# Kernel optimization log

Measured on AMD Instinct MI355X. Metric: run time of the kernel, lower is better.

The kernel has to match this reference:

```python
import jax, jax.numpy as jnp
import numpy as np
import math

B, C, H, W = 8, 512, 32, 32
NH = 8           # num_heads
G = 32           # group norm groups
EPS = 1e-6


def group_norm(x, gamma, beta, groups=G, eps=EPS):
    # x: [B, C, H, W]
    b, c, h, w = x.shape
    xr = x.reshape(b, groups, c // groups, h, w)
    mu = xr.mean(axis=(2, 3, 4), keepdims=True)
    var = xr.var(axis=(2, 3, 4), keepdims=True)
    xn = ((xr - mu) * jax.lax.rsqrt(var + eps)).reshape(b, c, h, w)
    return xn * gamma[None, :, None, None] + beta[None, :, None, None]


def conv2d(x, w, b, pad):
    y = jax.lax.conv_general_dilated(
        x, w, window_strides=(1, 1), padding=[(pad, pad), (pad, pad)],
        dimension_numbers=("NCHW", "OIHW", "NCHW"))
    return y + b[None, :, None, None]


def setup_inputs() -> dict:
    key = jax.random.key(0)
    ks = jax.random.split(key, 20)
    def n(k, shape, s=0.02):
        return jax.random.normal(k, shape, dtype=jnp.float32) * s
    f32 = jnp.float32
    return {
        "hidden_states": jax.random.normal(ks[0], (B, C, H, W), dtype=f32),
        "pre_g": jnp.ones(C, f32), "pre_b": jnp.zeros(C, f32),
        "norm_g": jnp.ones(C, f32), "norm_b": jnp.zeros(C, f32),
        "post_g": jnp.ones(C, f32), "post_b": jnp.zeros(C, f32),
        "pos_emb": n(ks[1], (1, C, 32, 32)),
        "wq": n(ks[2], (C, C)), "wk": n(ks[3], (C, C)), "wv": n(ks[4], (C, C)),
        "wq0": n(ks[5], (C // 2, C)), "wq1": n(ks[6], (C // 2, C)),
        "wk0": n(ks[7], (C // 2, C)), "wk1": n(ks[8], (C // 2, C)),
        "wv0": n(ks[9], (C // 2, C)), "wv1": n(ks[10], (C // 2, C)),
        "sa_w1": n(ks[11], (C // 8, C, 1, 1)), "sa_b1": jnp.zeros(C // 8, f32),
        "sa_w2": n(ks[12], (C // 8, C // 8, 3, 3)), "sa_b2": jnp.zeros(C // 8, f32),
        "sa_w3": n(ks[13], (1, C // 8, 1, 1)), "sa_b3": jnp.zeros(1, f32),
        "ff_w1": n(ks[14], (C, 2 * C)), "ff_b1": jnp.zeros(C, f32),
        "ff_w2": n(ks[15], (C, C)), "ff_b2": jnp.zeros(C, f32),
        "out_w": n(ks[16], (C, C)), "out_b": jnp.zeros(C, f32),
    }


def reference(hidden_states, pre_g, pre_b, norm_g, norm_b, post_g, post_b,
              pos_emb, wq, wk, wv, wq0, wq1, wk0, wk1, wv0, wv1,
              sa_w1, sa_b1, sa_w2, sa_b2, sa_w3, sa_b3,
              ff_w1, ff_b1, ff_w2, ff_b2, out_w, out_b):
    b, c, h, w = hidden_states.shape
    S = h * w
    residual = hidden_states
    x = group_norm(hidden_states, pre_g, pre_b)
    # H == W == 32: bilinear interpolation of pos_emb to its own size is identity
    x = x + pos_emb
    # conv-based sigmoid spatial gate
    s1 = jax.nn.silu(conv2d(x, sa_w1, sa_b1, 0))
    s2 = jax.nn.silu(conv2d(s1, sa_w2, sa_b2, 1))
    spatial_weights = jax.nn.sigmoid(conv2d(s2, sa_w3, sa_b3, 0))  # [B,1,H,W]
    spatial_enhanced = x * spatial_weights
    # standard attention path (self-attention: encoder states = normed tokens)
    sh = group_norm(x, norm_g, norm_b).reshape(b, c, S).transpose(0, 2, 1)  # [B,S,C]
    enc = sh
    hd = c // NH
    def split_heads(t):
        return t.reshape(b, S, NH, hd).transpose(0, 2, 1, 3)  # [B,NH,S,hd]
    qh = split_heads(sh @ wq.T)
    kh = split_heads(enc @ wk.T)
    vh = split_heads(enc @ wv.T)
    scores = jnp.einsum("bhqd,bhkd->bhqk", qh, kh) / math.sqrt(hd)
    probs = jax.nn.softmax(scores, axis=-1)
    standard_out = jnp.einsum("bhqk,bhkd->bhqd", probs, vh)
    standard_out = standard_out.transpose(0, 2, 1, 3).reshape(b, S, c)
    # multi-scale attention paths over the spatially gated features (single head)
    msh = spatial_enhanced.reshape(b, c, S).transpose(0, 2, 1)  # [B,S,C]
    parts = []
    for wqm, wkm, wvm in ((wq0, wk0, wv0), (wq1, wk1, wv1)):
        qm = msh @ wqm.T      # [B,S,C/2]
        km = enc @ wkm.T
        vm = enc @ wvm.T
        sc = jnp.einsum("bqd,bkd->bqk", qm, km) / math.sqrt(qm.shape[-1])
        parts.append(jnp.einsum("bqk,bkd->bqd", jax.nn.softmax(sc, axis=-1), vm))
    multi_out = jnp.concatenate(parts, axis=-1)            # [B,S,C]
    combined = jnp.concatenate([standard_out, multi_out], axis=-1)  # [B,S,2C]
    fused = jax.nn.silu(combined @ ff_w1.T + ff_b1) @ ff_w2.T + ff_b2  # dropout = eval
    final = fused @ out_w.T + out_b
    final = final.transpose(0, 2, 1).reshape(b, c, h, w)
    final = group_norm(final, post_g, post_b)
    return final + residual
```

## Files before the change

kernel.cpp:

```cpp
#include <hip/hip_runtime.h>

typedef unsigned short u16;
typedef unsigned long long u64;
typedef __attribute__((ext_vector_type(8))) short s8v;
typedef __attribute__((ext_vector_type(4))) short s4v;
typedef __attribute__((ext_vector_type(4))) float f4v;

#define LOG2E 1.4426950408889634f

__device__ __forceinline__ float b2f(u16 u) {
  union { unsigned u; float f; } x; x.u = ((unsigned)u) << 16; return x.f;
}
__device__ __forceinline__ u16 f2b(float f) {
  union { float f; unsigned u; } x; x.f = f;
  unsigned r = x.u + 0x7fffu + ((x.u >> 16) & 1u);
  return (u16)(r >> 16);
}
__device__ __forceinline__ unsigned cvtpk(float lo, float hi) {
  unsigned r;
  asm("v_cvt_pk_bf16_f32 %0, %1, %2" : "=v"(r) : "v"(lo), "v"(hi));
  return r;
}

#define MFMA16(a, b, c) __builtin_amdgcn_mfma_f32_16x16x32_bf16((a), (b), (c), 0, 0, 0)

__device__ __forceinline__ void gload16(const void* g, void* l) {
  __builtin_amdgcn_global_load_lds(
      (const __attribute__((address_space(1))) unsigned*)g,
      (__attribute__((address_space(3))) unsigned*)l, 16, 0, 0);
}

struct Segs {
  const float* src[14];
  int cum[15];
  float scl[14];
};

__global__ __launch_bounds__(256) void castk(Segs sg, u16* __restrict__ dst) {
  int gid = (blockIdx.x * 256 + threadIdx.x) * 4;
  if (gid >= sg.cum[14]) return;
  int s = 0;
  while (gid >= sg.cum[s + 1]) ++s;
  const float* sp = sg.src[s] + (gid - sg.cum[s]);
  float sc = sg.scl[s];
  f4v v = *(const f4v*)sp;
  s4v o;
  o[0] = (short)f2b(v[0] * sc); o[1] = (short)f2b(v[1] * sc);
  o[2] = (short)f2b(v[2] * sc); o[3] = (short)f2b(v[3] * sc);
  *(s4v*)(dst + gid) = o;
}

__global__ __launch_bounds__(256) void gn1_k(
    const float* __restrict__ hs, const float* __restrict__ pg, const float* __restrict__ pb,
    const float* __restrict__ pos, float* __restrict__ x,
    float* __restrict__ mu2, float* __restrict__ rs2)
{
  int bid = blockIdx.x;
  int b = bid >> 5, g = bid & 31;
  int tid = threadIdx.x, l = tid & 63, w = tid >> 6;
  const float* src = hs + ((size_t)b * 512 + g * 16) * 1024;
  const float* pp = pos + (size_t)(g * 16) * 1024;
  float* dst = x + ((size_t)b * 512 + g * 16) * 1024;
  f4v vals[16];
  float sum = 0.f, sq = 0.f;
#pragma unroll
  for (int i = 0; i < 16; ++i) {
    int idx = tid + i * 256;
    vals[i] = *(const f4v*)(src + (size_t)idx * 4);
    f4v v = vals[i];
    sum += v[0] + v[1] + v[2] + v[3];
    sq += v[0] * v[0] + v[1] * v[1] + v[2] * v[2] + v[3] * v[3];
  }
  __shared__ float red[8];
#pragma unroll
  for (int off = 1; off < 64; off <<= 1) { sum += __shfl_xor(sum, off); sq += __shfl_xor(sq, off); }
  if (l == 0) { red[w * 2] = sum; red[w * 2 + 1] = sq; }
  __syncthreads();
  float S = red[0] + red[2] + red[4] + red[6];
  float Q = red[1] + red[3] + red[5] + red[7];
  float mean = S * (1.f / 16384.f);
  float var = Q * (1.f / 16384.f) - mean * mean;
  float rstd = rsqrtf(var + 1e-6f);
  __syncthreads();
  float sum2 = 0.f, sq2 = 0.f;
#pragma unroll
  for (int i = 0; i < 16; ++i) {
    int idx = tid + i * 256;
    int c = idx >> 8;
    float gam = pg[g * 16 + c], bet = pb[g * 16 + c];
    f4v v = vals[i];
    f4v pe = *(const f4v*)(pp + (size_t)idx * 4);
    f4v o;
#pragma unroll
    for (int j = 0; j < 4; ++j) o[j] = (v[j] - mean) * rstd * gam + bet + pe[j];
    *(f4v*)(dst + (size_t)idx * 4) = o;
    sum2 += o[0] + o[1] + o[2] + o[3];
    sq2 += o[0] * o[0] + o[1] * o[1] + o[2] * o[2] + o[3] * o[3];
  }
#pragma unroll
  for (int off = 1; off < 64; off <<= 1) { sum2 += __shfl_xor(sum2, off); sq2 += __shfl_xor(sq2, off); }
  if (l == 0) { red[w * 2] = sum2; red[w * 2 + 1] = sq2; }
  __syncthreads();
  if (tid == 0) {
    float S2 = red[0] + red[2] + red[4] + red[6];
    float Q2 = red[1] + red[3] + red[5] + red[7];
    float m2 = S2 * (1.f / 16384.f);
    float v2 = Q2 * (1.f / 16384.f) - m2 * m2;
    mu2[b * 32 + g] = m2;
    rs2[b * 32 + g] = rsqrtf(v2 + 1e-6f);
  }
}

__global__ __launch_bounds__(256) void trans_gn2(
    const float* __restrict__ x, const float* __restrict__ mu2, const float* __restrict__ rs2,
    const float* __restrict__ ng, const float* __restrict__ nb,
    u16* __restrict__ xt, u16* __restrict__ sh)
{
  __shared__ float lds[512 * 17];
  int st = blockIdx.x, b = blockIdx.y;
  int tid = threadIdx.x;
  const float* xp = x + (size_t)b * 512 * 1024 + st * 16;
#pragma unroll
  for (int i = 0; i < 8; ++i) {
    int idx = tid + i * 256;
    int c = idx >> 2, sq = idx & 3;
    f4v v = *(const f4v*)(xp + (size_t)c * 1024 + sq * 4);
#pragma unroll
    for (int j = 0; j < 4; ++j) lds[c * 17 + sq * 4 + j] = v[j];
  }
  __syncthreads();
  int s = tid & 15, cb0 = (tid >> 4) * 32;
  size_t token = (size_t)b * 1024 + st * 16 + s;
  float m0 = mu2[b * 32 + (cb0 >> 4)], m1 = mu2[b * 32 + (cb0 >> 4) + 1];
  float r0 = rs2[b * 32 + (cb0 >> 4)], r1 = rs2[b * 32 + (cb0 >> 4) + 1];
#pragma unroll
  for (int q = 0; q < 4; ++q) {
    s8v ox, os;
#pragma unroll
    for (int j = 0; j < 8; ++j) {
      int cj = q * 8 + j;
      int c = cb0 + cj;
      float v = lds[c * 17 + s];
      ox[j] = (short)f2b(v);
      float mm = (cj < 16) ? m0 : m1;
      float rr = (cj < 16) ? r0 : r1;
      os[j] = (short)f2b((v - mm) * rr * ng[c] + nb[c]);
    }
    *(s8v*)(xt + token * 512 + cb0 + q * 8) = ox;
    *(s8v*)(sh + token * 512 + cb0 + q * 8) = os;
  }
}

template <int BM, int BN, bool SILU, bool OUT32, bool BIAS>
__global__ __launch_bounds__(256, 2) void gemm_k(
    const u16* __restrict__ A, int lda,
    const u16* __restrict__ Bw, int ldb,
    void* __restrict__ Cp, int ldc,
    const float* __restrict__ bias, int K, int ntx)
{
  constexpr int WMT = BM / 2, WNT = BN / 2, MF = WMT / 16, NF = WNT / 16;
  __shared__ u16 Al[BM * 64];
  __shared__ u16 Bl[BN * 64];
  const int tid = threadIdx.x, l = tid & 63, w = tid >> 6;
  const int lg = l >> 4, lr = l & 15;
  const int wm = w >> 1, wn = w & 1;
  const int flat = blockIdx.x;
  const int cpx = gridDim.x >> 3;
  const int id = (flat & 7) * cpx + (flat >> 3);
  const int grp = id / (ntx * 4), rem = id % (ntx * 4);
  const int nt = rem >> 2, mt = grp * 4 + (rem & 3);
  const u16* Ag = A + (size_t)mt * BM * lda;
  const u16* Bg = Bw + (size_t)nt * BN * ldb;
  const f4v z = {0.f, 0.f, 0.f, 0.f};
  f4v acc[MF][NF];
#pragma unroll
  for (int i = 0; i < MF; ++i)
#pragma unroll
    for (int j = 0; j < NF; ++j) acc[i][j] = z;

  for (int kt = 0; kt < K; kt += 64) {
    __syncthreads();
    for (int f = tid; f < BM * 8; f += 256) {
      int row = f >> 3, g = (f & 7) ^ (row & 7);
      gload16(Ag + (size_t)row * lda + kt + g * 8, (char*)Al + f * 16);
    }
    for (int f = tid; f < BN * 8; f += 256) {
      int row = f >> 3, g = (f & 7) ^ (row & 7);
      gload16(Bg + (size_t)row * ldb + kt + g * 8, (char*)Bl + f * 16);
    }
    __syncthreads();
#pragma unroll
    for (int ks = 0; ks < 2; ++ks) {
      s8v af[MF], bf[NF];
#pragma unroll
      for (int mf = 0; mf < MF; ++mf) {
        int row = wm * WMT + mf * 16 + lr;
        af[mf] = *(const s8v*)((const char*)Al + row * 128 + (((ks * 4 + lg) ^ (row & 7)) << 4));
      }
#pragma unroll
      for (int nf = 0; nf < NF; ++nf) {
        int row = wn * WNT + nf * 16 + lr;
        bf[nf] = *(const s8v*)((const char*)Bl + row * 128 + (((ks * 4 + lg) ^ (row & 7)) << 4));
      }
#pragma unroll
      for (int mf = 0; mf < MF; ++mf)
#pragma unroll
        for (int nf = 0; nf < NF; ++nf)
          acc[mf][nf] = MFMA16(af[mf], bf[nf], acc[mf][nf]);
    }
  }
#pragma unroll
  for (int mf = 0; mf < MF; ++mf) {
    int row0 = mt * BM + wm * WMT + mf * 16 + lg * 4;
#pragma unroll
    for (int nf = 0; nf < NF; ++nf) {
      int col = nt * BN + wn * WNT + nf * 16 + lr;
      float bv = BIAS ? bias[col] : 0.f;
#pragma unroll
      for (int r = 0; r < 4; ++r) {
        float v = acc[mf][nf][r] + bv;
        if (SILU) v = v / (1.f + exp2f(-v * LOG2E));
        size_t off = (size_t)(row0 + r) * ldc + col;
        if (OUT32) ((float*)Cp)[off] = v;
        else ((u16*)Cp)[off] = f2b(v);
      }
    }
  }
}

__global__ __launch_bounds__(256) void im2col_k(const u16* __restrict__ s1t, u16* __restrict__ col) {
  int gid = blockIdx.x * 256 + threadIdx.x;
  if (gid >= 8192 * 64) return;
  int token = gid >> 6, c = gid & 63;
  int s = token & 1023, y = s >> 5, xx = s & 31;
  u16* dst = col + (size_t)token * 576 + c * 9;
#pragma unroll
  for (int dy = 0; dy < 3; ++dy)
#pragma unroll
    for (int dx = 0; dx < 3; ++dx) {
      int yy = y + dy - 1, x2 = xx + dx - 1;
      u16 v = 0;
      if (yy >= 0 && yy < 32 && x2 >= 0 && x2 < 32)
        v = s1t[(size_t)(token + (dy - 1) * 32 + (dx - 1)) * 64 + c];
      dst[dy * 3 + dx] = v;
    }
}

__global__ __launch_bounds__(256) void conv3_k(
    const u16* __restrict__ s2t, const float* __restrict__ w3,
    const float* __restrict__ b3, float* __restrict__ gate)
{
  int token = blockIdx.x * 256 + threadIdx.x;
  if (token >= 8192) return;
  float acc = b3[0];
#pragma unroll
  for (int q = 0; q < 8; ++q) {
    s8v v = *(const s8v*)(s2t + (size_t)token * 64 + q * 8);
#pragma unroll
    for (int e = 0; e < 8; ++e) acc += b2f((u16)v[e]) * w3[q * 8 + e];
  }
  gate[token] = 1.f / (1.f + exp2f(-acc * LOG2E));
}

__global__ __launch_bounds__(256) void mshk(
    const u16* __restrict__ xt, const float* __restrict__ gate, u16* __restrict__ msh)
{
  int gid = blockIdx.x * 256 + threadIdx.x;
  if (gid >= 8192 * 64) return;
  int token = gid >> 6, j = gid & 63;
  float gt = gate[token];
  s8v v = *(const s8v*)(xt + (size_t)token * 512 + j * 8);
  s8v o;
#pragma unroll
  for (int e = 0; e < 8; ++e) o[e] = (short)f2b(b2f((u16)v[e]) * gt);
  *(s8v*)(msh + (size_t)token * 512 + j * 8) = o;
}

template <int HD>
__global__ __launch_bounds__(256) void tv_k(const u16* __restrict__ proj, int col0,
                                            u16* __restrict__ out)
{
  __shared__ u16 tile[64][HD + 2];
  const int tid = threadIdx.x;
  const int kb = blockIdx.x, y = blockIdx.y;
  const int nh = 512 / HD;
  const int b = y / nh, hh = y % nh;
  const u16* src = proj + ((size_t)b * 1024 + kb * 64) * 2560 + col0 + hh * HD;
  for (int f = tid; f < 64 * HD / 8; f += 256) {
    int key = f / (HD / 8), c = f % (HD / 8);
    *(s8v*)&tile[key][c * 8] = *(const s8v*)(src + (size_t)key * 2560 + c * 8);
  }
  __syncthreads();
  u16* dst = out + (size_t)y * HD * 1024 + kb * 64;
  for (int idx = tid; idx < HD * 16; idx += 256) {
    int d = idx >> 4, a = idx & 15;
    u16 e0 = tile[a][d], e1 = tile[16 + a][d], e2 = tile[32 + a][d], e3 = tile[48 + a][d];
    u64 v = (u64)e0 | ((u64)e1 << 16) | ((u64)e2 << 32) | ((u64)e3 << 48);
    *(u64*)(dst + (size_t)d * 1024 + a * 4) = v;
  }
}

__global__ __launch_bounds__(256, 4) void attn_std(
    const u16* __restrict__ proj, const u16* __restrict__ vts, u16* __restrict__ comb)
{
  const int tid = threadIdx.x, l = tid & 63, w = tid >> 6;
  const int lg = l >> 4, lr = l & 15;
  const int flat = blockIdx.x;
  const int xcd = flat & 7, idx = flat >> 3;
  const int bh = xcd + 8 * (idx >> 4);
  const int qt = idx & 15;
  const int b = bh >> 3, h = bh & 7;
  const size_t tokb = (size_t)b * 1024;
  __shared__ u16 Kl[2][64 * 64];
  __shared__ u16 Vl[2][64 * 64];
  __shared__ u16 Pl[4][16 * 64];
  const int qr0 = qt * 64 + w * 16;
  s8v qf[2];
#pragma unroll
  for (int ks = 0; ks < 2; ++ks)
    qf[ks] = *(const s8v*)(proj + (tokb + qr0 + lr) * 2560 + h * 64 + ks * 32 + lg * 8);
  const f4v z = {0.f, 0.f, 0.f, 0.f};
  f4v acc[4];
  float lsl[4] = {0.f, 0.f, 0.f, 0.f};
#pragma unroll
  for (int r = 0; r < 4; ++r) acc[r] = z;
  const u16* vbase = vts + (size_t)bh * 64 * 1024;

  auto stage = [&](int buf, int kt) {
    for (int f = tid; f < 512; f += 256) {
      int key = f >> 3, g = (f & 7) ^ (key & 7);
      gload16(proj + (tokb + kt * 64 + key) * 2560 + 512 + h * 64 + g * 8,
              (char*)&Kl[buf][0] + f * 16);
    }
    for (int f = tid; f < 512; f += 256) {
      int d = f >> 3, c = (f & 7) ^ (d & 7);
      gload16(vbase + (size_t)d * 1024 + kt * 64 + c * 8, (char*)&Vl[buf][0] + f * 16);
    }
  };

  stage(0, 0);
  __syncthreads();
  int cur = 0;
  for (int kt = 0; kt < 16; ++kt) {
    if (kt < 15) stage(cur ^ 1, kt + 1);
    f4v sf[4];
#pragma unroll
    for (int nf = 0; nf < 4; ++nf) sf[nf] = z;
#pragma unroll
    for (int ks = 0; ks < 2; ++ks) {
      s8v kfr[4];
#pragma unroll
      for (int nf = 0; nf < 4; ++nf) {
        int row = nf * 16 + lr;
        kfr[nf] = *(const s8v*)((const char*)&Kl[cur][0] + row * 128 + (((ks * 4 + lg) ^ (row & 7)) << 4));
      }
#pragma unroll
      for (int nf = 0; nf < 4; ++nf) sf[nf] = MFMA16(qf[ks], kfr[nf], sf[nf]);
    }
#pragma unroll
    for (int r = 0; r < 4; ++r) {
      float pv[4];
#pragma unroll
      for (int nf = 0; nf < 4; ++nf) pv[nf] = exp2f(sf[nf][r]);
      lsl[r] += (pv[0] + pv[1]) + (pv[2] + pv[3]);
      int q = lg * 4 + r;
      u64 pk = (u64)cvtpk(pv[0], pv[1]) | ((u64)cvtpk(pv[2], pv[3]) << 32);
      *(u64*)((char*)&Pl[w][0] + q * 128 + ((((lr >> 1) ^ (q & 7)) << 4)) + (lr & 1) * 8) = pk;
    }
#pragma unroll
    for (int ks2 = 0; ks2 < 2; ++ks2) {
      int g = ks2 * 4 + lg;
      s8v pfr = *(const s8v*)((const char*)&Pl[w][0] + lr * 128 + ((g ^ (lr & 7)) << 4));
#pragma unroll
      for (int nf = 0; nf < 4; ++nf) {
        int d = nf * 16 + lr;
        s8v vfr = *(const s8v*)((const char*)&Vl[cur][0] + d * 128 + ((g ^ (d & 7)) << 4));
        acc[nf] = MFMA16(pfr, vfr, acc[nf]);
      }
    }
    __syncthreads();
    cur ^= 1;
  }
#pragma unroll
  for (int r = 0; r < 4; ++r) {
    float t = lsl[r];
#pragma unroll
    for (int off = 1; off < 16; off <<= 1) t += __shfl_xor(t, off);
    float inv = 1.f / t;
    size_t row = tokb + qr0 + lg * 4 + r;
#pragma unroll
    for (int nf = 0; nf < 4; ++nf)
      comb[row * 1024 + h * 64 + nf * 16 + lr] = f2b(acc[nf][r] * inv);
  }
}

__global__ __launch_bounds__(256, 2) void attn_ms(
    const u16* __restrict__ proj, const u16* __restrict__ qm, const u16* __restrict__ vtm,
    u16* __restrict__ pacc, float* __restrict__ pl)
{
  const int tid = threadIdx.x, l = tid & 63, w = tid >> 6;
  const int lg = l >> 4, lr = l & 15;
  const int flat = blockIdx.x;
  const int xcd = flat & 7, idx = flat >> 3;
  const int bp = xcd + 8 * (idx >> 5);
  const int rest = idx & 31;
  const int qt = rest >> 1, ks = rest & 1;
  const int b = bp >> 1, p = bp & 1;
  const size_t tokb = (size_t)b * 1024;
  __shared__ u16 Kl[64 * 256];
  __shared__ u16 Vl[256 * 64];
  __shared__ u16 Pl[4][16 * 64];
  const int qr0 = qt * 64 + w * 16;
  s8v qf[8];
#pragma unroll
  for (int kf = 0; kf < 8; ++kf)
    qf[kf] = *(const s8v*)(qm + (tokb + qr0 + lr) * 512 + p * 256 + kf * 32 + lg * 8);
  const f4v z = {0.f, 0.f, 0.f, 0.f};
  f4v acc[16];
#pragma unroll
  for (int i = 0; i < 16; ++i) acc[i] = z;
  float lsl[4] = {0.f, 0.f, 0.f, 0.f};
  const u16* vbase = vtm + (size_t)bp * 256 * 1024;

  for (int kk = 0; kk < 8; ++kk) {
    const int key0 = ks * 512 + kk * 64;
    __syncthreads();
    for (int f = tid; f < 2048; f += 256) {
      int key = f >> 5, pgc = f & 31;
      int g = (pgc & 24) | ((pgc & 7) ^ (key & 7));
      gload16(proj + (tokb + key0 + key) * 2560 + 1536 + p * 256 + g * 8, (char*)Kl + f * 16);
    }
    for (int f = tid; f < 2048; f += 256) {
      int d = f >> 3, c = (f & 7) ^ (d & 7);
      gload16(vbase + (size_t)d * 1024 + key0 + c * 8, (char*)Vl + f * 16);
    }
    __syncthreads();
    f4v sf[4];
#pragma unroll
    for (int nf = 0; nf < 4; ++nf) sf[nf] = z;
#pragma unroll
    for (int ksi = 0; ksi < 8; ++ksi) {
      s8v kfr[4];
#pragma unroll
      for (int nf = 0; nf < 4; ++nf) {
        int row = nf * 16 + lr;
        int g = ksi * 4 + lg;
        int pg2 = (g & 24) | ((g & 7) ^ (row & 7));
        kfr[nf] = *(const s8v*)((const char*)Kl + row * 512 + (pg2 << 4));
      }
#pragma unroll
      for (int nf = 0; nf < 4; ++nf) sf[nf] = MFMA16(qf[ksi], kfr[nf], sf[nf]);
    }
#pragma unroll
    for (int r = 0; r < 4; ++r) {
      float pv[4];
#pragma unroll
      for (int nf = 0; nf < 4; ++nf) pv[nf] = exp2f(sf[nf][r]);
      lsl[r] += (pv[0] + pv[1]) + (pv[2] + pv[3]);
      int q = lg * 4 + r;
      u64 pk = (u64)cvtpk(pv[0], pv[1]) | ((u64)cvtpk(pv[2], pv[3]) << 32);
      *(u64*)((char*)&Pl[w][0] + q * 128 + ((((lr >> 1) ^ (q & 7)) << 4)) + (lr & 1) * 8) = pk;
    }
#pragma unroll
    for (int ks2 = 0; ks2 < 2; ++ks2) {
      int g = ks2 * 4 + lg;
      s8v pfr = *(const s8v*)((const char*)&Pl[w][0] + lr * 128 + ((g ^ (lr & 7)) << 4));
#pragma unroll
      for (int nfd = 0; nfd < 16; ++nfd) {
        int d = nfd * 16 + lr;
        s8v vfr = *(const s8v*)((const char*)Vl + d * 128 + ((g ^ (d & 7)) << 4));
        acc[nfd] = MFMA16(pfr, vfr, acc[nfd]);
      }
    }
  }
#pragma unroll
  for (int r = 0; r < 4; ++r) {
    float t = lsl[r];
#pragma unroll
    for (int off = 1; off < 16; off <<= 1) t += __shfl_xor(t, off);
    size_t prow = ((size_t)(bp * 2 + ks) * 16 + qt) * 64 + w * 16 + lg * 4 + r;
#pragma unroll
    for (int nfd = 0; nfd < 16; ++nfd)
      pacc[prow * 256 + nfd * 16 + lr] = f2b(acc[nfd][r]);
    if (lr == 0) pl[prow] = t;
  }
}

__global__ __launch_bounds__(256) void ms_comb(
    const u16* __restrict__ pacc, const float* __restrict__ pl,
    u16* __restrict__ comb)
{
  const int qt = blockIdx.x, bp = blockIdx.y;
  const int tid = threadIdx.x;
  const int row = tid >> 2, seg = tid & 3;
  size_t prow0 = ((size_t)(bp * 2 + 0) * 16 + qt) * 64 + row;
  size_t prow1 = ((size_t)(bp * 2 + 1) * 16 + qt) * 64 + row;
  float inv = 1.f / (pl[prow0] + pl[prow1]);
  const int b = bp >> 1, p = bp & 1;
  size_t orow = ((size_t)b * 1024 + qt * 64 + row) * 1024 + 512 + p * 256 + seg * 64;
#pragma unroll
  for (int j = 0; j < 8; ++j) {
    s8v v0 = *(const s8v*)(pacc + prow0 * 256 + seg * 64 + j * 8);
    s8v v1 = *(const s8v*)(pacc + prow1 * 256 + seg * 64 + j * 8);
    s8v ov;
#pragma unroll
    for (int e = 0; e < 8; ++e)
      ov[e] = (short)f2b((b2f((u16)v0[e]) + b2f((u16)v1[e])) * inv);
    *(s8v*)(comb + orow + j * 8) = ov;
  }
}

__global__ __launch_bounds__(256) void gn3_stats(
    const float* __restrict__ fin, float* __restrict__ mu3, float* __restrict__ rs3)
{
  int bid = blockIdx.x;
  int b = bid >> 5, g = bid & 31;
  int tid = threadIdx.x, l = tid & 63, w = tid >> 6;
  const float* fp = fin + (size_t)b * 1024 * 512 + g * 16;
  float sum = 0.f, sq = 0.f;
#pragma unroll
  for (int i = 0; i < 16; ++i) {
    int idx = tid + i * 256;
    int s = idx >> 2, cq = idx & 3;
    f4v v = *(const f4v*)(fp + (size_t)s * 512 + cq * 4);
    sum += v[0] + v[1] + v[2] + v[3];
    sq += v[0] * v[0] + v[1] * v[1] + v[2] * v[2] + v[3] * v[3];
  }
  __shared__ float red[8];
#pragma unroll
  for (int off = 1; off < 64; off <<= 1) { sum += __shfl_xor(sum, off); sq += __shfl_xor(sq, off); }
  if (l == 0) { red[w * 2] = sum; red[w * 2 + 1] = sq; }
  __syncthreads();
  if (tid == 0) {
    float S = red[0] + red[2] + red[4] + red[6];
    float Q = red[1] + red[3] + red[5] + red[7];
    float mean = S * (1.f / 16384.f);
    float var = Q * (1.f / 16384.f) - mean * mean;
    mu3[b * 32 + g] = mean;
    rs3[b * 32 + g] = rsqrtf(var + 1e-6f);
  }
}

__global__ __launch_bounds__(256) void final_k(
    const float* __restrict__ fin, const float* __restrict__ mu3, const float* __restrict__ rs3,
    const float* __restrict__ postg, const float* __restrict__ postb,
    const float* __restrict__ res, float* __restrict__ out)
{
  __shared__ float lds[16 * 513];
  int st = blockIdx.x, b = blockIdx.y;
  int tid = threadIdx.x;
  const float* fp = fin + ((size_t)b * 1024 + st * 16) * 512;
#pragma unroll
  for (int i = 0; i < 8; ++i) {
    int idx = tid + i * 256;
    int s = idx >> 7, cq = idx & 127;
    f4v v = *(const f4v*)(fp + (size_t)s * 512 + cq * 4);
#pragma unroll
    for (int j = 0; j < 4; ++j) lds[s * 513 + cq * 4 + j] = v[j];
  }
  __syncthreads();
#pragma unroll
  for (int cc = 0; cc < 2; ++cc) {
    int c = tid * 2 + cc;
    int g = c >> 4;
    float m = mu3[b * 32 + g], rv = rs3[b * 32 + g];
    float ga = postg[c], be = postb[c];
    const float* rp = res + ((size_t)b * 512 + c) * 1024 + st * 16;
    float* op = out + ((size_t)b * 512 + c) * 1024 + st * 16;
#pragma unroll
    for (int q = 0; q < 4; ++q) {
      f4v rr = *(const f4v*)(rp + q * 4);
      f4v o;
#pragma unroll
      for (int j = 0; j < 4; ++j) {
        float v = lds[(q * 4 + j) * 513 + c];
        o[j] = (v - m) * rv * ga + be + rr[j];
      }
      *(f4v*)(op + q * 4) = o;
    }
  }
}

extern "C" void kernel_launch(void* const* d_in, const int* in_sizes, int n_in,
                              void* d_out, int out_size, void* d_ws, size_t ws_size,
                              hipStream_t stream) {
  (void)in_sizes; (void)n_in; (void)out_size; (void)ws_size;
  const float* hs     = (const float*)d_in[0];
  const float* pre_g  = (const float*)d_in[1];
  const float* pre_b  = (const float*)d_in[2];
  const float* norm_g = (const float*)d_in[3];
  const float* norm_b = (const float*)d_in[4];
  const float* post_g = (const float*)d_in[5];
  const float* post_b = (const float*)d_in[6];
  const float* pos    = (const float*)d_in[7];
  const float* sa_b1  = (const float*)d_in[18];
  const float* sa_b2  = (const float*)d_in[20];
  const float* sa_w3  = (const float*)d_in[21];
  const float* sa_b3  = (const float*)d_in[22];
  const float* ff_b1  = (const float*)d_in[24];
  const float* ff_b2  = (const float*)d_in[26];
  const float* out_b  = (const float*)d_in[28];

  char* ws = (char*)d_ws;
  size_t off = 0;
  auto alloc = [&](size_t bytes) -> void* {
    void* pp = ws + off;
    off += (bytes + 255) & ~(size_t)255;
    return pp;
  };
  float* x    = (float*)alloc((size_t)16777216);
  u16* sh     = (u16*)alloc((size_t)8388608);
  u16* xt     = (u16*)alloc((size_t)8388608);
  float* mu2  = (float*)alloc(1024);
  float* rs2  = (float*)alloc(1024);
  float* mu3  = (float*)alloc(1024);
  float* rs3  = (float*)alloc(1024);
  float* pl   = (float*)alloc(262144);
  u16* wcat   = (u16*)alloc((size_t)2691072 * 2);
  u16* proj   = (u16*)alloc((size_t)8192 * 2560 * 2);
  u16* qmb    = (u16*)alloc((size_t)8388608);
  u16* s1t    = (u16*)alloc((size_t)1048576);
  u16* colb   = (u16*)alloc((size_t)8192 * 576 * 2);
  u16* s2t    = (u16*)alloc((size_t)1048576);
  float* gate = (float*)alloc((size_t)32768);
  u16* msh    = (u16*)alloc((size_t)8388608);
  u16* comb   = (u16*)alloc((size_t)16777216);
  u16* f1     = (u16*)alloc((size_t)8388608);
  u16* f2     = (u16*)alloc((size_t)8388608);
  float* fin  = x;
  u16* pacc   = (u16*)x;
  u16* vts    = colb;
  u16* vtm    = msh;

  u16* Wbig = wcat;
  u16* Wq01 = wcat + 1310720;
  u16* W1   = wcat + 1572864;
  u16* W2   = wcat + 1605632;
  u16* Wff1 = wcat + 1642496;
  u16* Wff2 = wcat + 2166784;
  u16* Wout = wcat + 2428928;

  Segs sg;
  const int srcidx[14] = {8, 9, 10, 13, 14, 15, 16, 11, 12, 17, 19, 23, 25, 27};
  const int segsz[14] = {262144, 262144, 262144, 131072, 131072, 131072, 131072,
                         131072, 131072, 32768, 36864, 524288, 262144, 262144};
  int cum = 0;
  for (int i = 0; i < 14; ++i) {
    sg.src[i] = (const float*)d_in[srcidx[i]];
    sg.cum[i] = cum;
    sg.scl[i] = 1.f;
    cum += segsz[i];
  }
  sg.cum[14] = cum;
  sg.scl[0] = 0.125f * LOG2E;
  sg.scl[7] = 0.0625f * LOG2E;
  sg.scl[8] = 0.0625f * LOG2E;

  dim3 blk(256);
  castk<<<2628, blk, 0, stream>>>(sg, wcat);
  gn1_k<<<256, blk, 0, stream>>>(hs, pre_g, pre_b, pos, x, mu2, rs2);
  trans_gn2<<<dim3(64, 8), blk, 0, stream>>>(x, mu2, rs2, norm_g, norm_b, xt, sh);
  gemm_k<128, 128, false, false, false><<<1280, blk, 0, stream>>>(
      sh, 512, Wbig, 512, proj, 2560, nullptr, 512, 20);
  gemm_k<64, 64, true, false, true><<<128, blk, 0, stream>>>(
      xt, 512, W1, 512, s1t, 64, sa_b1, 512, 1);
  im2col_k<<<2048, blk, 0, stream>>>(s1t, colb);
  gemm_k<64, 64, true, false, true><<<128, blk, 0, stream>>>(
      colb, 576, W2, 576, s2t, 64, sa_b2, 576, 1);
  conv3_k<<<32, blk, 0, stream>>>(s2t, sa_w3, sa_b3, gate);
  mshk<<<2048, blk, 0, stream>>>(xt, gate, msh);
  gemm_k<128, 64, false, false, false><<<512, blk, 0, stream>>>(
      msh, 512, Wq01, 512, qmb, 512, nullptr, 512, 8);
  tv_k<64><<<dim3(16, 64), blk, 0, stream>>>(proj, 1024, vts);
  tv_k<256><<<dim3(16, 16), blk, 0, stream>>>(proj, 2048, vtm);
  attn_std<<<1024, blk, 0, stream>>>(proj, vts, comb);
  attn_ms<<<512, blk, 0, stream>>>(proj, qmb, vtm, pacc, pl);
  ms_comb<<<dim3(16, 16), blk, 0, stream>>>(pacc, pl, comb);
  gemm_k<128, 64, true, false, true><<<512, blk, 0, stream>>>(
      comb, 1024, Wff1, 1024, f1, 512, ff_b1, 1024, 8);
  gemm_k<128, 64, false, false, true><<<512, blk, 0, stream>>>(
      f1, 512, Wff2, 512, f2, 512, ff_b2, 512, 8);
  gemm_k<128, 64, false, true, true><<<512, blk, 0, stream>>>(
      f2, 512, Wout, 512, fin, 512, out_b, 512, 8);
  gn3_stats<<<256, blk, 0, stream>>>(fin, mu3, rs3);
  final_k<<<dim3(64, 8), blk, 0, stream>>>(fin, mu3, rs3, post_g, post_b, hs, (float*)d_out);
}
```

Before: 259.4 us.

## Store pre-norm activations as bf16 and precompute attention staging pointers

The first group-norm kernel now writes its output as bf16 instead of fp32, and the transpose/second-norm kernel reads bf16, halving that intermediate's traffic. Separately, both attention kernels precompute per-thread global and LDS addresses for K/V staging and advance them incrementally instead of recomputing index math each tile. The bf16 intermediate adds rounding before the transpose, and xt/sh values now derive from rounded data, a slight numerical change; the second-stage statistics are still computed from fp32 values.

After: 256.6 us. Within noise of the previous version (-1.1%).

```diff
diff --git a/kernel.cpp b/kernel.cpp
--- a/kernel.cpp
+++ b/kernel.cpp
@@ -52,7 +52,7 @@
 
 __global__ __launch_bounds__(256) void gn1_k(
     const float* __restrict__ hs, const float* __restrict__ pg, const float* __restrict__ pb,
-    const float* __restrict__ pos, float* __restrict__ x,
+    const float* __restrict__ pos, u16* __restrict__ xb,
     float* __restrict__ mu2, float* __restrict__ rs2)
 {
   int bid = blockIdx.x;
@@ -60,7 +60,7 @@
   int tid = threadIdx.x, l = tid & 63, w = tid >> 6;
   const float* src = hs + ((size_t)b * 512 + g * 16) * 1024;
   const float* pp = pos + (size_t)(g * 16) * 1024;
-  float* dst = x + ((size_t)b * 512 + g * 16) * 1024;
+  u16* dst = xb + ((size_t)b * 512 + g * 16) * 1024;
   f4v vals[16];
   float sum = 0.f, sq = 0.f;
 #pragma unroll
@@ -91,9 +91,13 @@
     f4v v = vals[i];
     f4v pe = *(const f4v*)(pp + (size_t)idx * 4);
     f4v o;
-#pragma unroll
-    for (int j = 0; j < 4; ++j) o[j] = (v[j] - mean) * rstd * gam + bet + pe[j];
-    *(f4v*)(dst + (size_t)idx * 4) = o;
+    s4v ob;
+#pragma unroll
+    for (int j = 0; j < 4; ++j) {
+      o[j] = (v[j] - mean) * rstd * gam + bet + pe[j];
+      ob[j] = (short)f2b(o[j]);
+    }
+    *(s4v*)(dst + (size_t)idx * 4) = ob;
     sum2 += o[0] + o[1] + o[2] + o[3];
     sq2 += o[0] * o[0] + o[1] * o[1] + o[2] * o[2] + o[3] * o[3];
   }
@@ -112,21 +116,21 @@
 }
 
 __global__ __launch_bounds__(256) void trans_gn2(
-    const float* __restrict__ x, const float* __restrict__ mu2, const float* __restrict__ rs2,
+    const u16* __restrict__ xb, const float* __restrict__ mu2, const float* __restrict__ rs2,
     const float* __restrict__ ng, const float* __restrict__ nb,
     u16* __restrict__ xt, u16* __restrict__ sh)
 {
   __shared__ float lds[512 * 17];
   int st = blockIdx.x, b = blockIdx.y;
   int tid = threadIdx.x;
-  const float* xp = x + (size_t)b * 512 * 1024 + st * 16;
-#pragma unroll
-  for (int i = 0; i < 8; ++i) {
+  const u16* xp = xb + (size_t)b * 512 * 1024 + st * 16;
+#pragma unroll
+  for (int i = 0; i < 4; ++i) {
     int idx = tid + i * 256;
-    int c = idx >> 2, sq = idx & 3;
-    f4v v = *(const f4v*)(xp + (size_t)c * 1024 + sq * 4);
-#pragma unroll
-    for (int j = 0; j < 4; ++j) lds[c * 17 + sq * 4 + j] = v[j];
+    int c = idx >> 1, sq = (idx & 1) * 8;
+    s8v v = *(const s8v*)(xp + (size_t)c * 1024 + sq);
+#pragma unroll
+    for (int j = 0; j < 8; ++j) lds[c * 17 + sq + j] = b2f((u16)v[j]);
   }
   __syncthreads();
   int s = tid & 15, cb0 = (tid >> 4) * 32;
@@ -324,25 +328,37 @@
   float lsl[4] = {0.f, 0.f, 0.f, 0.f};
 #pragma unroll
   for (int r = 0; r < 4; ++r) acc[r] = z;
-  const u16* vbase = vts + (size_t)bh * 64 * 1024;
-
-  auto stage = [&](int buf, int kt) {
-    for (int f = tid; f < 512; f += 256) {
-      int key = f >> 3, g = (f & 7) ^ (key & 7);
-      gload16(proj + (tokb + kt * 64 + key) * 2560 + 512 + h * 64 + g * 8,
-              (char*)&Kl[buf][0] + f * 16);
-    }
-    for (int f = tid; f < 512; f += 256) {
-      int d = f >> 3, c = (f & 7) ^ (d & 7);
-      gload16(vbase + (size_t)d * 1024 + kt * 64 + c * 8, (char*)&Vl[buf][0] + f * 16);
-    }
+
+  const u16* gk[2];
+  const u16* gv[2];
+  char* lk[2];
+  char* lv[2];
+#pragma unroll
+  for (int j = 0; j < 2; ++j) {
+    int f = tid + j * 256;
+    int key = f >> 3, g = (f & 7) ^ (key & 7);
+    gk[j] = proj + (tokb + key) * 2560 + 512 + h * 64 + g * 8;
+    int c = (f & 7) ^ (key & 7);
+    gv[j] = vts + (size_t)bh * 64 * 1024 + (size_t)key * 1024 + c * 8;
+    lk[j] = (char*)&Kl[0][0] + f * 16;
+    lv[j] = (char*)&Vl[0][0] + f * 16;
+  }
+
+  auto stage = [&](int buf) {
+#pragma unroll
+    for (int j = 0; j < 2; ++j) {
+      gload16(gk[j], lk[j] + buf * 8192);
+      gload16(gv[j], lv[j] + buf * 8192);
+    }
+#pragma unroll
+    for (int j = 0; j < 2; ++j) { gk[j] += 64 * 2560; gv[j] += 64; }
   };
 
-  stage(0, 0);
+  stage(0);
   __syncthreads();
   int cur = 0;
   for (int kt = 0; kt < 16; ++kt) {
-    if (kt < 15) stage(cur ^ 1, kt + 1);
+    if (kt < 15) stage(cur ^ 1);
     f4v sf[4];
 #pragma unroll
     for (int nf = 0; nf < 4; ++nf) sf[nf] = z;
@@ -422,18 +438,26 @@
   float lsl[4] = {0.f, 0.f, 0.f, 0.f};
   const u16* vbase = vtm + (size_t)bp * 256 * 1024;
 
+  const u16* gk[8];
+  const u16* gv[8];
+#pragma unroll
+  for (int j = 0; j < 8; ++j) {
+    int f = tid + j * 256;
+    int key = f >> 5, pgc = f & 31;
+    int g = (pgc & 24) | ((pgc & 7) ^ (key & 7));
+    gk[j] = proj + (tokb + ks * 512 + key) * 2560 + 1536 + p * 256 + g * 8;
+    int d = f >> 3, c = (f & 7) ^ (d & 7);
+    gv[j] = vbase + (size_t)d * 1024 + ks * 512 + c * 8;
+  }
+
   for (int kk = 0; kk < 8; ++kk) {
-    const int key0 = ks * 512 + kk * 64;
     __syncthreads();
-    for (int f = tid; f < 2048; f += 256) {
-      int key = f >> 5, pgc = f & 31;
-      int g = (pgc & 24) | ((pgc & 7) ^ (key & 7));
-      gload16(proj + (tokb + key0 + key) * 2560 + 1536 + p * 256 + g * 8, (char*)Kl + f * 16);
-    }
-    for (int f = tid; f < 2048; f += 256) {
-      int d = f >> 3, c = (f & 7) ^ (d & 7);
-      gload16(vbase + (size_t)d * 1024 + key0 + c * 8, (char*)Vl + f * 16);
-    }
+#pragma unroll
+    for (int j = 0; j < 8; ++j) gload16(gk[j], (char*)Kl + (tid + j * 256) * 16);
+#pragma unroll
+    for (int j = 0; j < 8; ++j) gload16(gv[j], (char*)Vl + (tid + j * 256) * 16);
+#pragma unroll
+    for (int j = 0; j < 8; ++j) { gk[j] += 64 * 2560; gv[j] += 64; }
     __syncthreads();
     f4v sf[4];
 #pragma unroll
@@ -628,6 +652,7 @@
   u16* f1     = (u16*)alloc((size_t)8388608);
   u16* f2     = (u16*)alloc((size_t)8388608);
   float* fin  = x;
+  u16* xb     = (u16*)x;
   u16* pacc   = (u16*)x;
   u16* vts    = colb;
   u16* vtm    = msh;
@@ -658,8 +683,8 @@
 
   dim3 blk(256);
   castk<<<2628, blk, 0, stream>>>(sg, wcat);
-  gn1_k<<<256, blk, 0, stream>>>(hs, pre_g, pre_b, pos, x, mu2, rs2);
-  trans_gn2<<<dim3(64, 8), blk, 0, stream>>>(x, mu2, rs2, norm_g, norm_b, xt, sh);
+  gn1_k<<<256, blk, 0, stream>>>(hs, pre_g, pre_b, pos, xb, mu2, rs2);
+  trans_gn2<<<dim3(64, 8), blk, 0, stream>>>(xb, mu2, rs2, norm_g, norm_b, xt, sh);
   gemm_k<128, 128, false, false, false><<<1280, blk, 0, stream>>>(
       sh, 512, Wbig, 512, proj, 2560, nullptr, 512, 20);
   gemm_k<64, 64, true, false, true><<<128, blk, 0, stream>>>(
```
